# Optimization experiments

Measured on AMD Instinct MI355X. Metric: run time of the kernel, lower is better.

The kernel has to match this reference:

```python
import jax, jax.numpy as jnp
import numpy as np

T, B, DIM, N = 2, 256, 512, 196


def setup_inputs() -> dict:
    key = jax.random.key(0)
    ks = jax.random.split(key, 6)
    scale_mem = (2.0 / (DIM + DIM)) ** 0.5      # GlorotNormal
    scale_cat = (2.0 / (2 * DIM + DIM)) ** 0.5
    scale_attn = (2.0 / (DIM + 1)) ** 0.5
    return {
        "memory": jax.random.normal(ks[0], (T, B, DIM), dtype=jnp.float32),
        "know": jax.random.normal(ks[1], (B, DIM, N), dtype=jnp.float32),
        "control": jax.random.normal(ks[2], (T, B, DIM), dtype=jnp.float32),
        "W_mem": jax.random.normal(ks[3], (DIM, DIM), dtype=jnp.float32) * scale_mem,
        "b_mem": jnp.zeros((DIM,), dtype=jnp.float32),
        "W_concat": jax.random.normal(ks[4], (2 * DIM, DIM), dtype=jnp.float32) * scale_cat,
        "b_concat": jnp.zeros((DIM,), dtype=jnp.float32),
        "W_attn": jax.random.normal(ks[5], (DIM, 1), dtype=jnp.float32) * scale_attn,
        "b_attn": jnp.zeros((1,), dtype=jnp.float32),
    }


def reference(memory, know, control, W_mem, b_mem, W_concat, b_concat, W_attn, b_attn):
    # mem = Dense(dim)(memory[-1]) -> [B, dim]
    mem = memory[-1] @ W_mem + b_mem
    # mem[..., None] * know -> [B, dim, N]; concat along channel axis -> [B, 2*dim, N]
    cat = jnp.concatenate([mem[:, :, None] * know, know], axis=1)
    # transpose to [B, N, 2*dim], Dense(dim) -> [B, N, dim]
    concat = jnp.swapaxes(cat, 1, 2) @ W_concat + b_concat
    # gate by control[-1] -> [B, N, dim]; Dense(1) + squeeze -> [B, N]
    attn = concat * control[-1][:, None, :]
    logits = jnp.squeeze(attn @ W_attn, -1) + b_attn[0]
    # softmax over N, then (faithfully) weighted sum over the dim axis -> [B, N]
    a = jax.nn.softmax(logits, axis=1)[:, None, :]  # [B, 1, N]
    read = jnp.sum(a * know, axis=1)  # [B, N]
    return read
```

## Files before the change

kernel.cpp:

```cpp
#include <hip/hip_runtime.h>
#include <cfloat>

#define BB   256
#define DIM  512
#define NN   196

typedef __attribute__((ext_vector_type(8))) short bf16x8;
typedef __attribute__((ext_vector_type(4))) float f32x4;

__device__ __forceinline__ ushort f2bf(float x) {
    unsigned u = __float_as_uint(x);
    return (ushort)((u + 0x7FFFu + ((u >> 16) & 1u)) >> 16);
}

__device__ __forceinline__ bf16x8 pack8(float4 a, float4 b) {
    union { bf16x8 v; ushort u[8]; } r;
    r.u[0] = f2bf(a.x); r.u[1] = f2bf(a.y); r.u[2] = f2bf(a.z); r.u[3] = f2bf(a.w);
    r.u[4] = f2bf(b.x); r.u[5] = f2bf(b.y); r.u[6] = f2bf(b.z); r.u[7] = f2bf(b.w);
    return r.v;
}

__global__ __launch_bounds__(128) void prep_fused(
    const float* __restrict__ memory,
    const float* __restrict__ control,
    const float* __restrict__ W_mem,
    const float* __restrict__ b_mem,
    const float* __restrict__ W_concat,
    const float* __restrict__ W_attn,
    float* __restrict__ w_out)
{
    __shared__ __align__(16) ushort mus[2][16][520];

    const int tid = threadIdx.x;
    const int wv  = tid >> 6;
    const int l   = tid & 63;
    const int b0  = blockIdx.x * 16;
    const int i0  = blockIdx.y * 32;

    const float* mem_in = memory  + (size_t)BB * DIM;
    const float* ctl_in = control + (size_t)BB * DIM;

    #pragma unroll
    for (int p = 0; p < 32; ++p) {
        const int idx = p * 128 + tid;
        const int a   = idx >> 11;
        const int rb  = (idx >> 7) & 15;
        const int k4  = idx & 127;
        const float* src = a ? ctl_in : mem_in;
        float4 q = *(const float4*)&src[(size_t)(b0 + rb) * DIM + k4 * 4];
        if (a) {
            const float4 wa = ((const float4*)W_attn)[k4];
            q.x *= wa.x; q.y *= wa.y; q.z *= wa.z; q.w *= wa.w;
        }
        uint2 o;
        o.x = (unsigned)f2bf(q.x) | ((unsigned)f2bf(q.y) << 16);
        o.y = (unsigned)f2bf(q.z) | ((unsigned)f2bf(q.w) << 16);
        *(uint2*)&mus[a][rb][k4 * 4] = o;
    }
    __syncthreads();

    const int fr = l & 15;
    const int fk = (l >> 4) * 8;

    f32x4 accM = {0.f, 0.f, 0.f, 0.f};
    f32x4 acc1 = {0.f, 0.f, 0.f, 0.f};
    f32x4 acc2 = {0.f, 0.f, 0.f, 0.f};

    const int ib = i0 + wv * 16 + fr;
    const float* wmp = W_mem + ib;
    const float* c1p = W_concat + (size_t)ib * DIM;
    const float* c2p = W_concat + (size_t)(DIM + ib) * DIM;

    #pragma unroll 4
    for (int t = 0; t < 16; ++t) {
        const int k = t * 32 + fk;
        const bf16x8 am = *(const bf16x8*)&mus[0][fr][k];
        const bf16x8 au = *(const bf16x8*)&mus[1][fr][k];

        float wmv[8];
        #pragma unroll
        for (int j = 0; j < 8; ++j) wmv[j] = wmp[(size_t)(k + j) * DIM];
        union { bf16x8 v; ushort u[8]; } bm;
        #pragma unroll
        for (int j = 0; j < 8; ++j) bm.u[j] = f2bf(wmv[j]);

        const bf16x8 b1 = pack8(*(const float4*)&c1p[k],
                                *(const float4*)&c1p[k + 4]);
        const bf16x8 b2 = pack8(*(const float4*)&c2p[k],
                                *(const float4*)&c2p[k + 4]);

        accM = __builtin_amdgcn_mfma_f32_16x16x32_bf16(am, bm.v, accM, 0, 0, 0);
        acc1 = __builtin_amdgcn_mfma_f32_16x16x32_bf16(au, b1,   acc1, 0, 0, 0);
        acc2 = __builtin_amdgcn_mfma_f32_16x16x32_bf16(au, b2,   acc2, 0, 0, 0);
    }

    const float bmv = b_mem[ib];
    const int rb0 = (l >> 4) * 4;
    #pragma unroll
    for (int r = 0; r < 4; ++r) {
        w_out[(size_t)(b0 + rb0 + r) * DIM + ib] =
            (accM[r] + bmv) * acc1[r] + acc2[r];
    }
}

__global__ __launch_bounds__(1024) void read_kernel(
    const float* __restrict__ know,
    const float* __restrict__ w,
    float* __restrict__ out)
{
    __shared__ float  w_s[DIM];
    __shared__ float4 part_lg[16][50];
    __shared__ float4 part_ks[16][50];
    __shared__ float  tmp[256];
    __shared__ float  bc[2];

    const int tx  = threadIdx.x;
    const int ty  = threadIdx.y;
    const int tid = ty * 64 + tx;
    const int b   = blockIdx.x;

    if (tid < DIM) w_s[tid] = w[(size_t)b * DIM + tid];
    __syncthreads();

    float4 lg = make_float4(0.f, 0.f, 0.f, 0.f);
    float4 ks = make_float4(0.f, 0.f, 0.f, 0.f);
    if (tx < 49) {
        const float4* kp = (const float4*)(know + (size_t)b * DIM * NN) + (size_t)(ty * 32) * 49 + tx;
        const float*  wp = w_s + ty * 32;
        #pragma unroll 8
        for (int dd = 0; dd < 32; ++dd) {
            const float4 kv = kp[(size_t)dd * 49];
            const float  wv = wp[dd];
            lg.x = fmaf(kv.x, wv, lg.x); lg.y = fmaf(kv.y, wv, lg.y);
            lg.z = fmaf(kv.z, wv, lg.z); lg.w = fmaf(kv.w, wv, lg.w);
            ks.x += kv.x; ks.y += kv.y; ks.z += kv.z; ks.w += kv.w;
        }
        part_lg[ty][tx] = lg;
        part_ks[ty][tx] = ks;
    }
    __syncthreads();

    float lgn = 0.f, ksn = 0.f;
    if (tid < NN) {
        const int ng = tid >> 2, j = tid & 3;
        #pragma unroll
        for (int t = 0; t < 16; ++t) {
            lgn += ((const float*)&part_lg[t][ng])[j];
            ksn += ((const float*)&part_ks[t][ng])[j];
        }
    }

    if (tid < 256) tmp[tid] = (tid < NN) ? lgn : -FLT_MAX;
    __syncthreads();
    if (tid < 64) {
        float m = fmaxf(fmaxf(tmp[tid], tmp[tid + 64]),
                        fmaxf(tmp[tid + 128], tmp[tid + 192]));
        #pragma unroll
        for (int o = 32; o; o >>= 1) m = fmaxf(m, __shfl_down(m, o));
        if (tid == 0) bc[0] = m;
    }
    __syncthreads();

    const float e = (tid < NN) ? __expf(lgn - bc[0]) : 0.f;
    if (tid < 256) tmp[tid] = e;
    __syncthreads();
    if (tid < 64) {
        float s = tmp[tid] + tmp[tid + 64] + tmp[tid + 128] + tmp[tid + 192];
        #pragma unroll
        for (int o = 32; o; o >>= 1) s += __shfl_down(s, o);
        if (tid == 0) bc[1] = s;
    }
    __syncthreads();

    if (tid < NN) out[(size_t)b * NN + tid] = e / bc[1] * ksn;
}

extern "C" void kernel_launch(void* const* d_in, const int* in_sizes, int n_in,
                              void* d_out, int out_size, void* d_ws, size_t ws_size,
                              hipStream_t stream) {
    const float* memory   = (const float*)d_in[0];
    const float* know     = (const float*)d_in[1];
    const float* control  = (const float*)d_in[2];
    const float* W_mem    = (const float*)d_in[3];
    const float* b_mem    = (const float*)d_in[4];
    const float* W_concat = (const float*)d_in[5];
    const float* W_attn   = (const float*)d_in[7];
    float* w_ws = (float*)d_ws;
    float* outp = (float*)d_out;

    prep_fused<<<dim3(BB / 16, DIM / 32), dim3(128), 0, stream>>>(
        memory, control, W_mem, b_mem, W_concat, W_attn, w_ws);
    read_kernel<<<dim3(BB), dim3(64, 16), 0, stream>>>(know, w_ws, outp);
}
```

Before: 33.54 us.

## Split K across 8 waves in prep kernel with shared-memory reduction

The prep GEMM kernel goes from 128 to 512 threads per block. Each of the 8 waves now handles a 64-wide slice of the K dimension for both 16-column sub-tiles, instead of each wave running the full K loop. Partial MFMA accumulators are written to a 48KB shared buffer and reduced across waves before the epilogue. This shortens the serial K loop per wave and adds latency hiding, at the cost of extra LDS traffic, two more barriers and higher shared-memory use per block.

After: 30.11 us. -10.2%, faster.

```diff
diff --git a/kernel.cpp b/kernel.cpp
--- a/kernel.cpp
+++ b/kernel.cpp
@@ -20,7 +20,7 @@
     return r.v;
 }
 
-__global__ __launch_bounds__(128) void prep_fused(
+__global__ __launch_bounds__(512) void prep_fused(
     const float* __restrict__ memory,
     const float* __restrict__ control,
     const float* __restrict__ W_mem,
@@ -29,20 +29,20 @@
     const float* __restrict__ W_attn,
     float* __restrict__ w_out)
 {
-    __shared__ __align__(16) ushort mus[2][16][520];
+    __shared__ __align__(16) unsigned char smem[49152];
 
     const int tid = threadIdx.x;
-    const int wv  = tid >> 6;
-    const int l   = tid & 63;
     const int b0  = blockIdx.x * 16;
     const int i0  = blockIdx.y * 32;
 
+    ushort (*mus)[16][520] = (ushort (*)[16][520])smem;
+
     const float* mem_in = memory  + (size_t)BB * DIM;
     const float* ctl_in = control + (size_t)BB * DIM;
 
     #pragma unroll
-    for (int p = 0; p < 32; ++p) {
-        const int idx = p * 128 + tid;
+    for (int p = 0; p < 8; ++p) {
+        const int idx = p * 512 + tid;
         const int a   = idx >> 11;
         const int rb  = (idx >> 7) & 15;
         const int k4  = idx & 127;
@@ -59,47 +59,67 @@
     }
     __syncthreads();
 
+    const int wv = tid >> 6;
+    const int l  = tid & 63;
     const int fr = l & 15;
     const int fk = (l >> 4) * 8;
 
-    f32x4 accM = {0.f, 0.f, 0.f, 0.f};
-    f32x4 acc1 = {0.f, 0.f, 0.f, 0.f};
-    f32x4 acc2 = {0.f, 0.f, 0.f, 0.f};
-
-    const int ib = i0 + wv * 16 + fr;
-    const float* wmp = W_mem + ib;
-    const float* c1p = W_concat + (size_t)ib * DIM;
-    const float* c2p = W_concat + (size_t)(DIM + ib) * DIM;
-
-    #pragma unroll 4
-    for (int t = 0; t < 16; ++t) {
-        const int k = t * 32 + fk;
-        const bf16x8 am = *(const bf16x8*)&mus[0][fr][k];
-        const bf16x8 au = *(const bf16x8*)&mus[1][fr][k];
-
-        float wmv[8];
-        #pragma unroll
-        for (int j = 0; j < 8; ++j) wmv[j] = wmp[(size_t)(k + j) * DIM];
-        union { bf16x8 v; ushort u[8]; } bm;
-        #pragma unroll
-        for (int j = 0; j < 8; ++j) bm.u[j] = f2bf(wmv[j]);
-
-        const bf16x8 b1 = pack8(*(const float4*)&c1p[k],
-                                *(const float4*)&c1p[k + 4]);
-        const bf16x8 b2 = pack8(*(const float4*)&c2p[k],
-                                *(const float4*)&c2p[k + 4]);
-
-        accM = __builtin_amdgcn_mfma_f32_16x16x32_bf16(am, bm.v, accM, 0, 0, 0);
-        acc1 = __builtin_amdgcn_mfma_f32_16x16x32_bf16(au, b1,   acc1, 0, 0, 0);
-        acc2 = __builtin_amdgcn_mfma_f32_16x16x32_bf16(au, b2,   acc2, 0, 0, 0);
-    }
-
-    const float bmv = b_mem[ib];
+    f32x4 accM[2] = {{0.f,0.f,0.f,0.f}, {0.f,0.f,0.f,0.f}};
+    f32x4 acc1[2] = {{0.f,0.f,0.f,0.f}, {0.f,0.f,0.f,0.f}};
+    f32x4 acc2[2] = {{0.f,0.f,0.f,0.f}, {0.f,0.f,0.f,0.f}};
+
+    #pragma unroll
+    for (int s = 0; s < 2; ++s) {
+        const int ib = i0 + s * 16 + fr;
+        const float* wmp = W_mem + ib;
+        const float* c1p = W_concat + (size_t)ib * DIM;
+        const float* c2p = W_concat + (size_t)(DIM + ib) * DIM;
+        #pragma unroll
+        for (int ts = 0; ts < 2; ++ts) {
+            const int k = wv * 64 + ts * 32 + fk;
+            const bf16x8 am = *(const bf16x8*)&mus[0][fr][k];
+            const bf16x8 au = *(const bf16x8*)&mus[1][fr][k];
+            float wmv[8];
+            #pragma unroll
+            for (int j = 0; j < 8; ++j) wmv[j] = wmp[(size_t)(k + j) * DIM];
+            union { bf16x8 v; ushort u[8]; } bm;
+            #pragma unroll
+            for (int j = 0; j < 8; ++j) bm.u[j] = f2bf(wmv[j]);
+            const bf16x8 b1 = pack8(*(const float4*)&c1p[k],
+                                    *(const float4*)&c1p[k + 4]);
+            const bf16x8 b2 = pack8(*(const float4*)&c2p[k],
+                                    *(const float4*)&c2p[k + 4]);
+            accM[s] = __builtin_amdgcn_mfma_f32_16x16x32_bf16(am, bm.v, accM[s], 0, 0, 0);
+            acc1[s] = __builtin_amdgcn_mfma_f32_16x16x32_bf16(au, b1,   acc1[s], 0, 0, 0);
+            acc2[s] = __builtin_amdgcn_mfma_f32_16x16x32_bf16(au, b2,   acc2[s], 0, 0, 0);
+        }
+    }
+
+    __syncthreads();
+    float* P = (float*)smem;
     const int rb0 = (l >> 4) * 4;
     #pragma unroll
-    for (int r = 0; r < 4; ++r) {
-        w_out[(size_t)(b0 + rb0 + r) * DIM + ib] =
-            (accM[r] + bmv) * acc1[r] + acc2[r];
+    for (int s = 0; s < 2; ++s) {
+        #pragma unroll
+        for (int r = 0; r < 4; ++r) {
+            const int idx = (rb0 + r) * 32 + s * 16 + fr;
+            P[(0 * 8 + wv) * 512 + idx] = accM[s][r];
+            P[(1 * 8 + wv) * 512 + idx] = acc1[s][r];
+            P[(2 * 8 + wv) * 512 + idx] = acc2[s][r];
+        }
+    }
+    __syncthreads();
+    {
+        float sm = 0.f, v1 = 0.f, v2 = 0.f;
+        #pragma unroll
+        for (int c = 0; c < 8; ++c) {
+            sm += P[(0 * 8 + c) * 512 + tid];
+            v1 += P[(1 * 8 + c) * 512 + tid];
+            v2 += P[(2 * 8 + c) * 512 + tid];
+        }
+        const int bl = tid >> 5, il = tid & 31;
+        const int i  = i0 + il;
+        w_out[(size_t)(b0 + bl) * DIM + i] = (sm + b_mem[i]) * v1 + v2;
     }
 }
 
@@ -188,7 +208,7 @@
     float* w_ws = (float*)d_ws;
     float* outp = (float*)d_out;
 
-    prep_fused<<<dim3(BB / 16, DIM / 32), dim3(128), 0, stream>>>(
+    prep_fused<<<dim3(BB / 16, DIM / 32), dim3(512), 0, stream>>>(
         memory, control, W_mem, b_mem, W_concat, W_attn, w_ws);
     read_kernel<<<dim3(BB), dim3(64, 16), 0, stream>>>(know, w_ws, outp);
 }
```
